# Kernel optimization log

Hardware: AMD Instinct MI355X
Metric: run time of the kernel (lower is better)

## Reference

```python
import jax, jax.numpy as jnp
import numpy as np


def setup_inputs() -> dict:
    key = jax.random.key(0)
    k1, k2 = jax.random.split(key)
    N, D, C = 16384, 128, 1000
    embeddings = jax.random.normal(k1, (N, D), dtype=jnp.float32)
    labels = jax.random.randint(k2, (N,), 0, C, dtype=jnp.int64)
    return {"embeddings": embeddings, "labels": labels}


def reference(embeddings, labels):
    # Vectorized equivalent of the O(N^2) Python mining loop:
    # for each anchor i, positive = first j>i with labels[j]==labels[i],
    #                    negative = first j>i with labels[j]!=labels[i].
    # Anchor i yields a triplet only if BOTH exist.
    # Original returns a variable-length stack; for fixed shapes we return the
    # full [3, N, D] triplets (invalid anchors zeroed) plus a validity mask.
    N = labels.shape[0]
    same = labels[:, None] == labels[None, :]            # [N, N]
    upper = jnp.arange(N)[None, :] > jnp.arange(N)[:, None]  # j > i
    pos_cand = same & upper
    neg_cand = (~same) & upper
    pos_idx = jnp.argmax(pos_cand, axis=1)               # first True (0 if none)
    neg_idx = jnp.argmax(neg_cand, axis=1)
    valid = pos_cand.any(axis=1) & neg_cand.any(axis=1)  # [N]
    triplets = jnp.stack([embeddings,
                          embeddings[pos_idx],
                          embeddings[neg_idx]])          # [3, N, D]
    triplets = triplets * valid[None, :, None].astype(embeddings.dtype)
    return triplets, valid
```

## Files before the change

### kernel.cpp

```cpp
#include <hip/hip_runtime.h>

typedef float f32x4 __attribute__((ext_vector_type(4)));

__global__ void __launch_bounds__(256) triplet_fused_kernel(
    const int* __restrict__ labels,
    const f32x4* __restrict__ emb,
    f32x4* __restrict__ out,
    float* __restrict__ valid_out,
    int N, int D4) {

    int lane = threadIdx.x & 63;
    int i = blockIdx.x * (blockDim.x >> 6) + (threadIdx.x >> 6);
    if (i >= N) return;

    int my = labels[i];
    const int4* lab4 = (const int4*)labels;
    int nq = N >> 2;

    int kbase = (i + 1) >> 2;
    int p = -1, ng = -1;

    int4 a0 = lab4[min(kbase +       lane, nq - 1)];
    int4 b0 = lab4[min(kbase +  64 + lane, nq - 1)];
    int4 a1 = lab4[min(kbase + 128 + lane, nq - 1)];
    int4 b1 = lab4[min(kbase + 192 + lane, nq - 1)];

    while (true) {
        int4 a2 = lab4[min(kbase + 256 + lane, nq - 1)];
        int4 b2 = lab4[min(kbase + 320 + lane, nq - 1)];

        unsigned msA = 0, mdA = 0, msB = 0, mdB = 0;
        int kqA = kbase + lane;
        int kqB = kbase + 64 + lane;
        if (kqA < nq) {
            int j0 = kqA << 2;
            if (j0 + 0 > i) { if (a0.x == my) msA |= 1u; else mdA |= 1u; }
            if (j0 + 1 > i) { if (a0.y == my) msA |= 2u; else mdA |= 2u; }
            if (j0 + 2 > i) { if (a0.z == my) msA |= 4u; else mdA |= 4u; }
            if (j0 + 3 > i) { if (a0.w == my) msA |= 8u; else mdA |= 8u; }
        }
        if (kqB < nq) {
            if (b0.x == my) msB |= 1u; else mdB |= 1u;
            if (b0.y == my) msB |= 2u; else mdB |= 2u;
            if (b0.z == my) msB |= 4u; else mdB |= 4u;
            if (b0.w == my) msB |= 8u; else mdB |= 8u;
        }

        unsigned long long bsA = __ballot(msA != 0);
        unsigned long long bdA = __ballot(mdA != 0);
        unsigned long long bsB = __ballot(msB != 0);
        unsigned long long bdB = __ballot(mdB != 0);

        if (p < 0) {
            if (bsA) {
                int ls = (int)__ffsll(bsA) - 1;
                unsigned m = __shfl(msA, ls);
                p = ((kbase + ls) << 2) + (__ffs(m) - 1);
            } else if (bsB) {
                int ls = (int)__ffsll(bsB) - 1;
                unsigned m = __shfl(msB, ls);
                p = ((kbase + 64 + ls) << 2) + (__ffs(m) - 1);
            }
        }
        if (ng < 0) {
            if (bdA) {
                int ls = (int)__ffsll(bdA) - 1;
                unsigned m = __shfl(mdA, ls);
                ng = ((kbase + ls) << 2) + (__ffs(m) - 1);
            } else if (bdB) {
                int ls = (int)__ffsll(bdB) - 1;
                unsigned m = __shfl(mdB, ls);
                ng = ((kbase + 64 + ls) << 2) + (__ffs(m) - 1);
            }
        }

        kbase += 128;
        if ((p >= 0 && ng >= 0) || kbase >= nq) break;
        a0 = a1; b0 = b1; a1 = a2; b1 = b2;
    }

    float v  = (p >= 0 && ng >= 0) ? 1.0f : 0.0f;
    int   ps = (p  >= 0) ? p  : 0;
    int   ns = (ng >= 0) ? ng : 0;

    if (lane == 0) valid_out[i] = v;

    size_t ND4 = (size_t)N * D4;
    int t   = lane >> 5;
    int src = (t == 0) ? i : ps;
    int d4  = lane & 31;

    f32x4 e = emb[(size_t)src * D4 + d4];
    f32x4 r; r.x = e.x * v; r.y = e.y * v; r.z = e.z * v; r.w = e.w * v;
    __builtin_nontemporal_store(r, &out[(size_t)t * ND4 + (size_t)i * D4 + d4]);

    if (lane < 32) {
        f32x4 e2 = emb[(size_t)ns * D4 + d4];
        f32x4 r2; r2.x = e2.x * v; r2.y = e2.y * v; r2.z = e2.z * v; r2.w = e2.w * v;
        __builtin_nontemporal_store(r2, &out[2 * ND4 + (size_t)i * D4 + d4]);
    }
}

extern "C" void kernel_launch(void* const* d_in, const int* in_sizes, int n_in,
                              void* d_out, int out_size, void* d_ws, size_t ws_size,
                              hipStream_t stream) {
    const float* emb    = (const float*)d_in[0];
    const int*   labels = (const int*)d_in[1];

    int N  = in_sizes[1];
    int D  = in_sizes[0] / N;
    int D4 = D / 4;

    float* out       = (float*)d_out;
    float* valid_out = out + (size_t)3 * N * D;

    const int block = 256;
    int anchors_per_block = block / 64;
    int nblk = (N + anchors_per_block - 1) / anchors_per_block;
    triplet_fused_kernel<<<nblk, block, 0, stream>>>(
        labels, (const f32x4*)emb, (f32x4*)out, valid_out, N, D4);
}
```

Before: 16.19 us.

## Stage full label array in LDS per block and widen blocks to 16 waves

```diff
diff --git a/kernel.cpp b/kernel.cpp
--- a/kernel.cpp
+++ b/kernel.cpp
@@ -2,32 +2,43 @@
 
 typedef float f32x4 __attribute__((ext_vector_type(4)));
 
-__global__ void __launch_bounds__(256) triplet_fused_kernel(
+#define WAVES_PER_BLOCK 16
+#define BLOCK (WAVES_PER_BLOCK * 64)
+
+__global__ void __launch_bounds__(BLOCK, 2) triplet_fused_kernel(
     const int* __restrict__ labels,
     const f32x4* __restrict__ emb,
     f32x4* __restrict__ out,
     float* __restrict__ valid_out,
     int N, int D4) {
 
+    __shared__ int4 slab4[4096];
+    const int4* lab4 = (const int4*)labels;
+    int nq = N >> 2;
+
+    for (int k = threadIdx.x; k < nq; k += BLOCK)
+        slab4[k] = lab4[k];
+    __syncthreads();
+
     int lane = threadIdx.x & 63;
-    int i = blockIdx.x * (blockDim.x >> 6) + (threadIdx.x >> 6);
+    int wid  = threadIdx.x >> 6;
+    int i    = blockIdx.x * WAVES_PER_BLOCK + wid;
     if (i >= N) return;
 
-    int my = labels[i];
-    const int4* lab4 = (const int4*)labels;
-    int nq = N >> 2;
+    const int* slab = (const int*)slab4;
+    int my = slab[i];
 
     int kbase = (i + 1) >> 2;
     int p = -1, ng = -1;
 
-    int4 a0 = lab4[min(kbase +       lane, nq - 1)];
-    int4 b0 = lab4[min(kbase +  64 + lane, nq - 1)];
-    int4 a1 = lab4[min(kbase + 128 + lane, nq - 1)];
-    int4 b1 = lab4[min(kbase + 192 + lane, nq - 1)];
+    int4 a0 = slab4[min(kbase +       lane, nq - 1)];
+    int4 b0 = slab4[min(kbase +  64 + lane, nq - 1)];
+    int4 a1 = slab4[min(kbase + 128 + lane, nq - 1)];
+    int4 b1 = slab4[min(kbase + 192 + lane, nq - 1)];
 
     while (true) {
-        int4 a2 = lab4[min(kbase + 256 + lane, nq - 1)];
-        int4 b2 = lab4[min(kbase + 320 + lane, nq - 1)];
+        int4 a2 = slab4[min(kbase + 256 + lane, nq - 1)];
+        int4 b2 = slab4[min(kbase + 320 + lane, nq - 1)];
 
         unsigned msA = 0, mdA = 0, msB = 0, mdB = 0;
         int kqA = kbase + lane;
@@ -114,9 +125,7 @@
     float* out       = (float*)d_out;
     float* valid_out = out + (size_t)3 * N * D;
 
-    const int block = 256;
-    int anchors_per_block = block / 64;
-    int nblk = (N + anchors_per_block - 1) / anchors_per_block;
-    triplet_fused_kernel<<<nblk, block, 0, stream>>>(
+    int nblk = (N + WAVES_PER_BLOCK - 1) / WAVES_PER_BLOCK;
+    triplet_fused_kernel<<<nblk, BLOCK, 0, stream>>>(
         labels, (const f32x4*)emb, (f32x4*)out, valid_out, N, D4);
 }
```

After: 18.46 us. +14.0%, slower.
